# Performance work log

Measured on AMD Instinct MI355X. Metric: run time of the kernel, lower is better.

## Reference

```python
import jax, jax.numpy as jnp
import numpy as np

B, S, HID = 2, 4096, 1024
H, D = 16, 64

def rotate_half(x):
    x1, x2 = jnp.split(x, 2, axis=-1)
    return jnp.concatenate([-x2, x1], axis=-1)

def setup_inputs() -> dict:
    key = jax.random.key(0)
    ks = jax.random.split(key, 8)
    hidden_states = jax.random.normal(ks[0], (B, S, HID), dtype=jnp.float32)
    pos = jnp.arange(S, dtype=jnp.float32)[:, None]
    inv_freq = 1.0 / (10000.0 ** (jnp.arange(0, D, 2, dtype=jnp.float32) / D))
    freqs = pos * inv_freq[None, :]
    emb = jnp.concatenate([freqs, freqs], axis=-1)  # [S, D]
    cos = jnp.cos(emb)
    sin = jnp.sin(emb)
    W_rkv = jax.random.normal(ks[1], (3 * H * D, HID), dtype=jnp.float32) * 0.02
    W_o = jax.random.normal(ks[2], (HID, H * D), dtype=jnp.float32) * 0.02
    # match torch init: uniform(-8,-5), uniform(-1,1), uniform(0.2,0.8)
    time_decay = jax.random.uniform(ks[3], (H, D), minval=-8.0, maxval=-5.0, dtype=jnp.float32)
    time_first = jax.random.uniform(ks[4], (H, D), minval=-1.0, maxval=1.0, dtype=jnp.float32)
    time_mix = jax.random.uniform(ks[5], (1, 1, HID), minval=0.2, maxval=0.8, dtype=jnp.float32)
    return {"hidden_states": hidden_states, "cos": cos, "sin": sin,
            "W_rkv": W_rkv, "W_o": W_o, "time_decay": time_decay,
            "time_first": time_first, "time_mix": time_mix}

def reference(hidden_states, cos, sin, W_rkv, W_o, time_decay, time_first, time_mix):
    b, s, hid = hidden_states.shape
    # token-shift time mixing
    xx = jnp.concatenate([jnp.zeros_like(hidden_states[:, :1]), hidden_states[:, :-1]], axis=1)
    mixed = hidden_states * time_mix + xx * (1.0 - time_mix)
    rkv = jnp.einsum('bsh,oh->bso', mixed, W_rkv).reshape(b, s, 3, H, D)
    r = jax.nn.sigmoid(rkv[:, :, 0])  # [B,S,H,D]
    k = rkv[:, :, 1]
    v = rkv[:, :, 2]
    # rotary on r, k
    c = cos[None, :, None, :]
    sn = sin[None, :, None, :]
    r = r * c + rotate_half(r) * sn
    k = k * c + rotate_half(k) * sn
    # fast rwkv linear attention (parallel approximation)
    w = -jnp.exp(time_decay)
    kv = k * v  # [B,S,H,D]
    pos = jnp.arange(s, dtype=hidden_states.dtype)
    pos_diff = pos[:, None] - pos[None, :]  # [S,S]
    mask = pos_diff > 0  # i > j masked (per original code)
    avg_decay = jnp.mean(w)
    pd = jnp.where(mask, 0.0, pos_diff)
    dw = jnp.where(mask, 0.0, jnp.exp(avg_decay * -jnp.abs(pd)))
    dw = dw / (dw.sum(axis=1, keepdims=True) + 1e-8)
    weighted_kv = jnp.einsum('ij,bjhd->bihd', dw, kv)
    out = r * (time_first[None, None] * kv + weighted_kv)  # [B,S,H,D]
    out = out.reshape(b, s, H * D)
    return jnp.einsum('bso,ho->bsh', out, W_o)
```

## Files before the change

kernel.cpp:

```cpp
#include <hip/hip_runtime.h>
#include <math.h>

#define S_LEN 4096
#define HIDN  1024
#define NH    16
#define HD    64
#define BATCH 2
#define M_TOTAL (BATCH * S_LEN)
#define N_RKV   (3 * HIDN)
#define CS 128
#define NC (S_LEN / CS)

typedef __attribute__((ext_vector_type(8))) _Float16 f16x8;
typedef __attribute__((ext_vector_type(4))) float f32x4;
typedef __attribute__((ext_vector_type(4))) unsigned short u16x4;

__device__ __forceinline__ unsigned short f2h(float x) {
    _Float16 h = (_Float16)x;
    return *(unsigned short*)&h;
}
__device__ __forceinline__ float h2f(unsigned short b) {
    _Float16 h = *(_Float16*)&b;
    return (float)h;
}

__device__ __forceinline__ void load_lds16(const void* g, void* l) {
    __builtin_amdgcn_global_load_lds((const __attribute__((address_space(1))) void*)g,
                                     (__attribute__((address_space(3))) void*)l, 16, 0, 0);
}

__global__ void k_avg_decay(const float* __restrict__ td, float* __restrict__ a_out) {
    int t = threadIdx.x;
    double acc = 0.0;
    for (int i = t; i < NH * HD; i += 64) acc += exp((double)td[i]);
    for (int off = 32; off > 0; off >>= 1) acc += __shfl_down(acc, off, 64);
    if (t == 0) a_out[0] = (float)(acc / (double)(NH * HD));
}

__global__ __launch_bounds__(256)
void k_split_mix(const float* __restrict__ hs, const float* __restrict__ tm,
                 unsigned short* __restrict__ Ah) {
    int g = blockIdx.x * 256 + threadIdx.x;
    int kc = (g & 255) * 4;
    int m = g >> 8;
    float4 cur = *(const float4*)&hs[(size_t)m * HIDN + kc];
    float4 t4  = *(const float4*)&tm[kc];
    float4 prev = make_float4(0.f, 0.f, 0.f, 0.f);
    if (m & (S_LEN - 1)) prev = *(const float4*)&hs[(size_t)(m - 1) * HIDN + kc];
    u16x4 h;
    h.x = f2h(cur.x * t4.x + prev.x * (1.f - t4.x));
    h.y = f2h(cur.y * t4.y + prev.y * (1.f - t4.y));
    h.z = f2h(cur.z * t4.z + prev.z * (1.f - t4.z));
    h.w = f2h(cur.w * t4.w + prev.w * (1.f - t4.w));
    *(u16x4*)&Ah[(size_t)m * HIDN + kc] = h;
}

__global__ __launch_bounds__(256)
void k_split_w(const float* __restrict__ W, unsigned short* __restrict__ Wh) {
    int g = blockIdx.x * 256 + threadIdx.x;
    size_t o = (size_t)g * 4;
    float4 v = *(const float4*)&W[o];
    u16x4 h;
    h.x = f2h(v.x); h.y = f2h(v.y); h.z = f2h(v.z); h.w = f2h(v.w);
    *(u16x4*)&Wh[o] = h;
}

__device__ __forceinline__ f32x4 mfma16(f16x8 a, f16x8 b, f32x4 c) {
    return __builtin_amdgcn_mfma_f32_16x16x32_f16(a, b, c, 0, 0, 0);
}

template<int LDC, int NBX, bool HALF_OUT>
__global__ __launch_bounds__(256, 2)
void k_gemm_bt(const unsigned short* __restrict__ A,
               const unsigned short* __restrict__ Bm,
               void* __restrict__ Cv)
{
    __shared__ unsigned short smem[16384];
    const int tid  = threadIdx.x;
    const int lane = tid & 63;
    const int wave = tid >> 6;
    const int wm = wave >> 1, wn = wave & 1;

    const int cpx = gridDim.x >> 3;
    const int wg  = (blockIdx.x & 7) * cpx + (blockIdx.x >> 3);
    const int bx  = wg % NBX;
    const int by  = wg / NBX;
    const int m0 = by * 128;
    const int n0 = bx * 128;

    const unsigned short* segsrc[4];
    int segdst[4];
    {
        int rowoff = lane >> 2;
        int q = (lane & 3) ^ (rowoff & 3);
#pragma unroll
        for (int i = 0; i < 4; ++i) {
            int s = wave * 4 + i;
            const unsigned short* base = (s < 8) ? A : Bm;
            int row = (s < 8) ? (m0 + s * 16) : (n0 + (s - 8) * 16);
            segsrc[i] = base + (size_t)(row + rowoff) * 1024 + q * 8;
            segdst[i] = s * 512;
        }
    }

    const int lm = lane & 15;
    const int rq = lane >> 4;
    const int qx = rq ^ (lane & 3);
    int aoff[4], boff[4];
#pragma unroll
    for (int t = 0; t < 4; ++t) {
        aoff[t] = (wm * 64 + t * 16 + lm) * 32 + qx * 8;
        boff[t] = 4096 + (wn * 64 + t * 16 + lm) * 32 + qx * 8;
    }

    f32x4 acc[4][4] = {};

#pragma unroll
    for (int i = 0; i < 4; ++i) load_lds16(segsrc[i], smem + segdst[i]);

    int p = 0;
    for (int kt = 0; kt < 1024; kt += 32) {
        __syncthreads();
        if (kt + 32 < 1024) {
#pragma unroll
            for (int i = 0; i < 4; ++i)
                load_lds16(segsrc[i] + kt + 32, smem + ((p ^ 1) * 8192 + segdst[i]));
        }
        const unsigned short* sb = smem + p * 8192;
        f16x8 fa[4], fb[4];
#pragma unroll
        for (int t = 0; t < 4; ++t) {
            fa[t] = *(const f16x8*)(sb + aoff[t]);
            fb[t] = *(const f16x8*)(sb + boff[t]);
        }
#pragma unroll
        for (int mt = 0; mt < 4; ++mt)
#pragma unroll
            for (int nt = 0; nt < 4; ++nt)
                acc[mt][nt] = mfma16(fa[mt], fb[nt], acc[mt][nt]);
        p ^= 1;
    }

#pragma unroll
    for (int mt = 0; mt < 4; ++mt)
#pragma unroll
        for (int nt = 0; nt < 4; ++nt) {
            int col = n0 + wn * 64 + nt * 16 + lm;
#pragma unroll
            for (int r = 0; r < 4; ++r) {
                int row = m0 + wm * 64 + mt * 16 + rq * 4 + r;
                if constexpr (HALF_OUT)
                    ((unsigned short*)Cv)[(size_t)row * LDC + col] = f2h(acc[mt][nt][r]);
                else
                    ((float*)Cv)[(size_t)row * LDC + col] = acc[mt][nt][r];
            }
        }
}

__global__ __launch_bounds__(256)
void k_cb(const unsigned short* __restrict__ rkv,
          const float* __restrict__ cosp, const float* __restrict__ sinp,
          const float* __restrict__ a_ptr, float* __restrict__ Cb)
{
    __shared__ float Ls[4][64][4];
    int bid = blockIdx.x;
    int c  = bid & (NC - 1);
    int bh = bid >> 5;
    int b = bh >> 4, h = bh & 15;
    int lane = threadIdx.x & 63;
    int wave = threadIdx.x >> 6;
    int lm = lane & 15;
    int rs = lane >> 4;
    int d0 = lm * 4;
    float a = a_ptr[0];
    float sgn = (lm < 8) ? -1.f : 1.f;
    float ps0 = 0.f, ps1 = 0.f, ps2 = 0.f, ps3 = 0.f;
#pragma unroll
    for (int it = 0; it < 8; ++it) {
        int t = wave * 32 + it * 4 + rs;
        int s = c * CS + t;
        const unsigned short* rk = rkv + ((size_t)b * S_LEN + s) * N_RKV + h * 64 + d0;
        u16x4 k4 = *(const u16x4*)(rk + 1024);
        u16x4 v4 = *(const u16x4*)(rk + 2048);
        float4 cs4 = *(const float4*)&cosp[s * HD + d0];
        float4 sn4 = *(const float4*)&sinp[s * HD + d0];
        float e = expf(a * (float)t);
        float k0 = h2f(k4.x), k1 = h2f(k4.y), k2 = h2f(k4.z), k3 = h2f(k4.w);
        float kp0 = __shfl_xor(k0, 8, 64);
        float kp1 = __shfl_xor(k1, 8, 64);
        float kp2 = __shfl_xor(k2, 8, 64);
        float kp3 = __shfl_xor(k3, 8, 64);
        ps0 += e * (k0 * cs4.x + sgn * kp0 * sn4.x) * h2f(v4.x);
        ps1 += e * (k1 * cs4.y + sgn * kp1 * sn4.y) * h2f(v4.y);
        ps2 += e * (k2 * cs4.z + sgn * kp2 * sn4.z) * h2f(v4.z);
        ps3 += e * (k3 * cs4.w + sgn * kp3 * sn4.w) * h2f(v4.w);
    }
    Ls[wave][lane][0] = ps0; Ls[wave][lane][1] = ps1;
    Ls[wave][lane][2] = ps2; Ls[wave][lane][3] = ps3;
    __syncthreads();
    if (threadIdx.x < 64) {
        int d = threadIdx.x;
        int lmm = d >> 2, j = d & 3;
        float sum = 0.f;
#pragma unroll
        for (int wv = 0; wv < 4; ++wv)
#pragma unroll
            for (int r = 0; r < 4; ++r)
                sum += Ls[wv][r * 16 + lmm][j];
        Cb[((size_t)bh * NC + c) * 64 + d] = sum;
    }
}

__global__ __launch_bounds__(64)
void k_chunk_suffix(const float* __restrict__ Cb, const float* __restrict__ a_ptr,
                    float* __restrict__ Sb) {
    int bh = blockIdx.x;
    int d = threadIdx.x;
    float a = a_ptr[0];
    float eaCS = expf(a * (float)CS);
    float run = 0.f;
    Sb[(size_t)(bh * NC + NC - 1) * 64 + d] = 0.f;
    for (int c = NC - 2; c >= 0; --c) {
        run = Cb[(size_t)(bh * NC + c + 1) * 64 + d] + eaCS * run;
        Sb[(size_t)(bh * NC + c) * 64 + d] = run;
    }
}

__global__ __launch_bounds__(256)
void k_wkv2(const unsigned short* __restrict__ rkv,
            const float* __restrict__ cosp, const float* __restrict__ sinp,
            const float* __restrict__ Sb, const float* __restrict__ a_ptr,
            const float* __restrict__ tf,
            unsigned short* __restrict__ outH) {
    __shared__ float Tl[4][64];
    int bid = blockIdx.x;
    int c  = bid & (NC - 1);
    int bh = bid >> 5;
    int b = bh >> 4, h = bh & 15;
    int lane = threadIdx.x & 63;
    int wave = threadIdx.x >> 6;
    float a = a_ptr[0];
    float ea = expf(a);
    float em1a = expm1f(a);
    int s0 = c * CS + wave * 32;
    const unsigned short* rkb = rkv + ((size_t)b * S_LEN + s0) * N_RKV + h * 64 + lane;
    float sgn = (lane < 32) ? -1.f : 1.f;

    float kvreg[32], rreg[32];
    float w = 1.f, T = 0.f;
#pragma unroll
    for (int t = 0; t < 32; ++t) {
        const unsigned short* pr = rkb + (size_t)t * N_RKV;
        float r_ = h2f(pr[0]);
        float k_ = h2f(pr[1024]);
        float v_ = h2f(pr[2048]);
        float cs = cosp[(s0 + t) * HD + lane];
        float sn = sinp[(s0 + t) * HD + lane];
        float sig = 1.f / (1.f + expf(-r_));
        float sigp = __shfl_xor(sig, 32, 64);
        float kp   = __shfl_xor(k_, 32, 64);
        rreg[t]  = sig * cs + sgn * sigp * sn;
        kvreg[t] = (k_ * cs + sgn * kp * sn) * v_;
        T += w * kvreg[t];
        w *= ea;
    }
    Tl[wave][lane] = T;
    __syncthreads();

    float e32 = expf(a * 32.f);
    float S_run = Sb[(size_t)bid * 64 + lane] * expf(a * 32.f * (float)(3 - wave));
    float f = 1.f;
    for (int wp = wave + 1; wp < 4; ++wp) {
        S_run += f * Tl[wp][lane];
        f *= e32;
    }
    float tfv = tf[h * HD + lane];
#pragma unroll
    for (int t = 31; t >= 0; --t) {
        float kv = kvreg[t];
        S_run = kv + ea * S_run;
        int ig = c * CS + wave * 32 + t;
        float Z = expm1f(a * (float)(S_LEN - ig)) / em1a + 1e-8f;
        float o = rreg[t] * (tfv * kv + S_run / Z);
        size_t m = (size_t)b * S_LEN + ig;
        outH[m * HIDN + h * HD + lane] = f2h(o);
    }
}

extern "C" void kernel_launch(void* const* d_in, const int* in_sizes, int n_in,
                              void* d_out, int out_size, void* d_ws, size_t ws_size,
                              hipStream_t stream) {
    const float* hs    = (const float*)d_in[0];
    const float* cosp  = (const float*)d_in[1];
    const float* sinp  = (const float*)d_in[2];
    const float* W_rkv = (const float*)d_in[3];
    const float* W_o   = (const float*)d_in[4];
    const float* td    = (const float*)d_in[5];
    const float* tf    = (const float*)d_in[6];
    const float* tm    = (const float*)d_in[7];
    float* out = (float*)d_out;

    char* w = (char*)d_ws;
    unsigned short* rkvH = (unsigned short*)w;
    unsigned short* Ah   = (unsigned short*)(w + 50331648);
    unsigned short* outH = (unsigned short*)(w + 50331648);
    unsigned short* Wrh  = (unsigned short*)(w + 67108864);
    unsigned short* Woh  = (unsigned short*)(w + 73400320);
    float*          Cb   = (float*)(w + 75497472);
    float*          Sb   = (float*)(w + 75759616);
    float*          a_ptr= (float*)(w + 76021760);

    k_avg_decay<<<1, 64, 0, stream>>>(td, a_ptr);

    k_split_mix<<<(M_TOTAL * HIDN / 4) / 256, 256, 0, stream>>>(hs, tm, Ah);
    k_split_w<<<(N_RKV * HIDN / 4) / 256, 256, 0, stream>>>(W_rkv, Wrh);
    k_split_w<<<(HIDN * HIDN / 4) / 256, 256, 0, stream>>>(W_o, Woh);

    k_gemm_bt<N_RKV, 24, true><<<1536, 256, 0, stream>>>(Ah, Wrh, rkvH);

    k_cb<<<BATCH * NH * NC, 256, 0, stream>>>(rkvH, cosp, sinp, a_ptr, Cb);
    k_chunk_suffix<<<BATCH * NH, 64, 0, stream>>>(Cb, a_ptr, Sb);
    k_wkv2<<<BATCH * NH * NC, 256, 0, stream>>>(rkvH, cosp, sinp, Sb, a_ptr, tf, outH);

    k_gemm_bt<HIDN, 8, false><<<512, 256, 0, stream>>>(outH, Woh, out);
}
```

Before: 254.2 us.

## Stage rkv chunk tiles in LDS and precompute normalizer table in WKV kernel

```diff
diff --git a/kernel.cpp b/kernel.cpp
--- a/kernel.cpp
+++ b/kernel.cpp
@@ -227,11 +227,22 @@
 }
 
 __global__ __launch_bounds__(256)
+void k_ztab(const float* __restrict__ a_ptr, float* __restrict__ Zt) {
+    int i = blockIdx.x * 256 + threadIdx.x;
+    if (i < S_LEN) {
+        float a = a_ptr[0];
+        float em1a = expm1f(a);
+        Zt[i] = expm1f(a * (float)(S_LEN - i)) / em1a + 1e-8f;
+    }
+}
+
+__global__ __launch_bounds__(256)
 void k_wkv2(const unsigned short* __restrict__ rkv,
             const float* __restrict__ cosp, const float* __restrict__ sinp,
             const float* __restrict__ Sb, const float* __restrict__ a_ptr,
-            const float* __restrict__ tf,
+            const float* __restrict__ tf, const float* __restrict__ Zt,
             unsigned short* __restrict__ outH) {
+    __shared__ unsigned short L[3 * 128 * 64];
     __shared__ float Tl[4][64];
     int bid = blockIdx.x;
     int c  = bid & (NC - 1);
@@ -239,26 +250,42 @@
     int b = bh >> 4, h = bh & 15;
     int lane = threadIdx.x & 63;
     int wave = threadIdx.x >> 6;
+    int s0 = c * CS;
+
+#pragma unroll
+    for (int i = 0; i < 12; ++i) {
+        int seg = wave * 12 + i;
+        int stream = seg >> 4;
+        int rg = seg & 15;
+        int row = rg * 8 + (lane >> 3);
+        const unsigned short* src = rkv
+            + ((size_t)b * S_LEN + s0 + row) * N_RKV + stream * 1024 + h * 64
+            + (lane & 7) * 8;
+        load_lds16(src, L + stream * 8192 + rg * 512);
+    }
+    __syncthreads();
+
     float a = a_ptr[0];
     float ea = expf(a);
-    float em1a = expm1f(a);
-    int s0 = c * CS + wave * 32;
-    const unsigned short* rkb = rkv + ((size_t)b * S_LEN + s0) * N_RKV + h * 64 + lane;
+    const unsigned short* Lr = L;
+    const unsigned short* Lk = L + 8192;
+    const unsigned short* Lv = L + 16384;
     float sgn = (lane < 32) ? -1.f : 1.f;
+    int lx = lane ^ 32;
 
     float kvreg[32], rreg[32];
     float w = 1.f, T = 0.f;
 #pragma unroll
     for (int t = 0; t < 32; ++t) {
-        const unsigned short* pr = rkb + (size_t)t * N_RKV;
-        float r_ = h2f(pr[0]);
-        float k_ = h2f(pr[1024]);
-        float v_ = h2f(pr[2048]);
-        float cs = cosp[(s0 + t) * HD + lane];
-        float sn = sinp[(s0 + t) * HD + lane];
+        int row = wave * 32 + t;
+        float r_ = h2f(Lr[row * 64 + lane]);
+        float k_ = h2f(Lk[row * 64 + lane]);
+        float kp = h2f(Lk[row * 64 + lx]);
+        float v_ = h2f(Lv[row * 64 + lane]);
+        float cs = cosp[(s0 + row) * HD + lane];
+        float sn = sinp[(s0 + row) * HD + lane];
         float sig = 1.f / (1.f + expf(-r_));
         float sigp = __shfl_xor(sig, 32, 64);
-        float kp   = __shfl_xor(k_, 32, 64);
         rreg[t]  = sig * cs + sgn * sigp * sn;
         kvreg[t] = (k_ * cs + sgn * kp * sn) * v_;
         T += w * kvreg[t];
@@ -279,8 +306,8 @@
     for (int t = 31; t >= 0; --t) {
         float kv = kvreg[t];
         S_run = kv + ea * S_run;
-        int ig = c * CS + wave * 32 + t;
-        float Z = expm1f(a * (float)(S_LEN - ig)) / em1a + 1e-8f;
+        int ig = s0 + wave * 32 + t;
+        float Z = Zt[ig];
         float o = rreg[t] * (tfv * kv + S_run / Z);
         size_t m = (size_t)b * S_LEN + ig;
         outH[m * HIDN + h * HD + lane] = f2h(o);
@@ -309,6 +336,7 @@
     float*          Cb   = (float*)(w + 75497472);
     float*          Sb   = (float*)(w + 75759616);
     float*          a_ptr= (float*)(w + 76021760);
+    float*          Zt   = Cb;
 
     k_avg_decay<<<1, 64, 0, stream>>>(td, a_ptr);
 
@@ -320,7 +348,8 @@
 
     k_cb<<<BATCH * NH * NC, 256, 0, stream>>>(rkvH, cosp, sinp, a_ptr, Cb);
     k_chunk_suffix<<<BATCH * NH, 64, 0, stream>>>(Cb, a_ptr, Sb);
-    k_wkv2<<<BATCH * NH * NC, 256, 0, stream>>>(rkvH, cosp, sinp, Sb, a_ptr, tf, outH);
+    k_ztab<<<S_LEN / 256, 256, 0, stream>>>(a_ptr, Zt);
+    k_wkv2<<<BATCH * NH * NC, 256, 0, stream>>>(rkvH, cosp, sinp, Sb, a_ptr, tf, Zt, outH);
 
     k_gemm_bt<HIDN, 8, false><<<512, 256, 0, stream>>>(outH, Woh, out);
 }
```

New measurement: 239.8 us. 5.7% less time.
